# Optimization experiments

Measured on AMD Instinct MI355X. Metric: run time of the kernel, lower is better.

Reference implementation:

```python
import jax, jax.numpy as jnp
import numpy as np

NMAX = 8
LMAX = 3
RC = 5.0
SIGMA = 0.5
SMOOTH_W = 0.5
N_SPECIES = 4
N_ATOMS = 20000
N_EDGES = 800000
LMMAX = (LMAX + 1) ** 2  # 16
# map each (l,m) flat index to its l (block structure of mult_ln_lm)
LM_TO_L = jnp.asarray(np.repeat(np.arange(LMAX + 1), 2 * np.arange(LMAX + 1) + 1))


def real_sph_harm_l3(d):
    """Real spherical harmonics, integral normalization, l=0..3. d: [J,3] unit vectors."""
    x, y, z = d[:, 0], d[:, 1], d[:, 2]
    x2, y2, z2 = x * x, y * y, z * z
    cols = [
        jnp.full_like(x, 0.28209479177387814),                 # l=0
        0.4886025119029199 * y,                                # l=1, m=-1
        0.4886025119029199 * z,                                # l=1, m=0
        0.4886025119029199 * x,                                # l=1, m=1
        1.0925484305920792 * x * y,                            # l=2, m=-2
        1.0925484305920792 * y * z,                            # l=2, m=-1
        0.31539156525252005 * (2.0 * z2 - x2 - y2),            # l=2, m=0
        1.0925484305920792 * x * z,                            # l=2, m=1
        0.5462742152960396 * (x2 - y2),                        # l=2, m=2
        0.5900435899266435 * y * (3.0 * x2 - y2),              # l=3, m=-3
        2.890611442640554 * x * y * z,                         # l=3, m=-2
        0.4570457994644658 * y * (4.0 * z2 - x2 - y2),         # l=3, m=-1
        0.3731763325901154 * z * (2.0 * z2 - 3.0 * x2 - 3.0 * y2),  # l=3, m=0
        0.4570457994644658 * x * (4.0 * z2 - x2 - y2),         # l=3, m=1
        1.445305721320277 * z * (x2 - y2),                     # l=3, m=2
        0.5900435899266435 * x * (x2 - 3.0 * y2),              # l=3, m=3
    ]
    return jnp.stack(cols, axis=-1)  # [J, 16]


def shifted_cosine_cutoff(r):
    """f=1 for r<rc-w, smooth cosine decay to 0 at rc, 0 beyond."""
    w = SMOOTH_W
    t = 0.5 * (1.0 + jnp.cos(jnp.pi * jnp.clip((r - (RC - w)) / w, 0.0, 1.0)))
    return jnp.where(r < RC - w, 1.0, jnp.where(r < RC, t, 0.0))


def setup_inputs() -> dict:
    key = jax.random.key(0)
    k1, k2, k3, k4, k5, k6 = jax.random.split(key, 6)
    distances = jax.random.uniform(k1, (N_EDGES,), jnp.float32, 0.05, RC * 0.999)
    dv = jax.random.normal(k2, (N_EDGES, 3), jnp.float32)
    direction_vectors = dv / jnp.linalg.norm(dv, axis=1, keepdims=True)
    radial_centers = jax.random.uniform(k3, ((LMAX + 1) * NMAX,), jnp.float32, 0.0, RC)
    z = jax.random.randint(k4, (N_ATOMS,), 0, N_SPECIES)
    idx_i = jax.random.randint(k5, (N_EDGES,), 0, N_ATOMS)
    idx_j = jax.random.randint(k6, (N_EDGES,), 0, N_ATOMS)
    return {"distances": distances, "direction_vectors": direction_vectors,
            "radial_centers": radial_centers, "z": z, "idx_i": idx_i, "idx_j": idx_j}


def reference(distances, direction_vectors, radial_centers, z, idx_i, idx_j):
    J = distances.shape[0]
    # spherical harmonics of edge directions: [J, lmmax]
    Ylm = real_sph_harm_l3(direction_vectors)
    # radial integrals (Gaussian-basis spline surrogate) * cutoff: [J, lmax+1, nmax]
    rb = jnp.exp(-0.5 * jnp.square((distances[:, None] - radial_centers[None, :]) / SIGMA))
    RIln = rb.reshape(J, LMAX + 1, NMAX) * shifted_cosine_cutoff(distances)[:, None, None]
    # block-wise outer product (vectorized mult_ln_lm): [J, nmax, lmmax]
    cij_nlm = RIln[:, LM_TO_L, :].transpose(0, 2, 1) * Ylm[:, None, :]
    # species- and atom-dependent scatter-add
    reduction_ids = z[idx_j] + N_SPECIES * idx_i
    ci = jax.ops.segment_sum(cij_nlm.reshape(J, -1), reduction_ids,
                             num_segments=N_SPECIES * N_ATOMS)
    return ci.reshape(N_ATOMS, N_SPECIES, NMAX, LMMAX)
```

## Files before the change

kernel.cpp:

```cpp
#include <hip/hip_runtime.h>
#include <math.h>


#define NSPEC 4
#define CAP   32

typedef float v2f __attribute__((ext_vector_type(2)));

__constant__ float YCOEF[16 * 20] = {
    0.28209479177387814f,0,0,0, 0,0,0,0, 0,0,0,0, 0,0,0,0, 0,0,0,0,
    0,0,0.4886025119029199f,0, 0,0,0,0, 0,0,0,0, 0,0,0,0, 0,0,0,0,
    0,0,0,0.4886025119029199f, 0,0,0,0, 0,0,0,0, 0,0,0,0, 0,0,0,0,
    0,0.4886025119029199f,0,0, 0,0,0,0, 0,0,0,0, 0,0,0,0, 0,0,0,0,
    0,0,0,0, 0,0,0,1.0925484305920792f, 0,0,0,0, 0,0,0,0, 0,0,0,0,
    0,0,0,0, 0,0,0,0, 0,1.0925484305920792f,0,0, 0,0,0,0, 0,0,0,0,
    0,0,0,0, -0.31539156525252005f,-0.31539156525252005f,0.6307831305050401f,0, 0,0,0,0, 0,0,0,0, 0,0,0,0,
    0,0,0,0, 0,0,0,0, 1.0925484305920792f,0,0,0, 0,0,0,0, 0,0,0,0,
    0,0,0,0, 0.5462742152960396f,-0.5462742152960396f,0,0, 0,0,0,0, 0,0,0,0, 0,0,0,0,
    0,0,0,0, 0,0,0,0, 0,0,0,1.7701307697799305f, 0,0,0,0, -0.5900435899266435f,0,0,0,
    0,0,0,0, 0,0,0,0, 0,0,0,0, 0,0,2.890611442640554f,0, 0,0,0,0,
    0,0,0,0, 0,0,0,0, 0,0,0,-0.4570457994644658f, 0,0,0,0, -0.4570457994644658f,0,1.8281831978578632f,0,
    0,0,0,0, 0,0,0,0, 0,0,0,0, -1.1195289977703462f,0,0,0, 0,-1.1195289977703462f,0,0.7463526651802308f,
    0,0,0,0, 0,0,0,0, 0,0,-0.4570457994644658f,0, 0,-0.4570457994644658f,0,1.8281831978578632f, 0,0,0,0,
    0,0,0,0, 0,0,0,0, 0,0,0,0, 1.445305721320277f,0,0,0, 0,-1.445305721320277f,0,0,
    0,0,0,0, 0,0,0,0, 0,0,0.5900435899266435f,0, 0,-1.7701307697799305f,0,0, 0,0,0,0,
};

__device__ __forceinline__ void gather_row(
    const float4* __restrict__ payload, const float* __restrict__ centers,
    float* __restrict__ out, int row, int lane, int beg, int end, int clampHi)
{
    int q = lane >> 4;
    int t = lane & 15;
    int l = (t >= 9) ? 3 : (t >= 4) ? 2 : (t >= 1) ? 1 : 0;
    float cenA = centers[2 * t];
    float cenB = centers[2 * t + 1];
    int srcA = (q << 4) + (l << 2);

    const float4* cr = (const float4*)(&YCOEF[t * 20]);
    float4 c0 = cr[0], c1 = cr[1], c2 = cr[2], c3 = cr[3], c4 = cr[4];
    v2f K0 = {c0.x, c0.y}, K1 = {c0.z, c0.w};
    v2f K2 = {c1.x, c1.y}, K3 = {c1.z, c1.w};
    v2f K4 = {c2.x, c2.y}, K5 = {c2.z, c2.w};
    v2f K6 = {c3.x, c3.y}, K7 = {c3.z, c3.w};
    v2f K8 = {c4.x, c4.y}, K9 = {c4.z, c4.w};
    asm volatile("" : "+v"(K0), "+v"(K1), "+v"(K2), "+v"(K3), "+v"(K4),
                      "+v"(K5), "+v"(K6), "+v"(K7), "+v"(K8), "+v"(K9),
                      "+v"(cenA), "+v"(cenB));

    v2f A0 = {0, 0}, A1 = {0, 0}, A2 = {0, 0}, A3 = {0, 0};

    if (beg < end) {
        float4 P = payload[beg];
        for (int i = beg; i < end; ++i) {
            int nx = i + 1 < clampHi ? i + 1 : clampHi;
            float4 Pn = payload[nx];
            float x = P.x, y = P.y, z = P.z, r = P.w;

            float xx = x * x, yy = y * y, zz = z * z;
            v2f m0 = {1.0f, x};
            v2f m1 = {y, z};
            v2f m2 = {xx, yy};
            v2f m3 = {zz, x * y};
            v2f m4 = {x * z, y * z};
            v2f m5 = {xx * x, xx * y};
            v2f m6 = {xx * z, x * yy};
            v2f m7 = {x * y * z, x * zz};
            v2f m8 = {yy * y, yy * z};
            v2f m9 = {y * zz, zz * z};

            v2f pa = K0 * m0 + K1 * m1;
            v2f pb = K2 * m2 + K3 * m3;
            pa += K4 * m4;
            pb += K5 * m5;
            pa += K6 * m6;
            pb += K7 * m7;
            pa += K8 * m8;
            pb += K9 * m9;
            v2f ps = pa + pb;
            float ylm = ps.x + ps.y;

            float u  = fminf(fmaxf((r - 4.5f) * 2.0f, 0.0f), 1.0f);
            float fc = fmaf(0.5f, __cosf(3.14159265358979f * u), 0.5f);
            float p  = fc * ylm;

            float dA = r - cenA;
            float dB = r - cenB;
            float rb0 = __expf(-2.0f * dA * dA);
            float rb1 = __expf(-2.0f * dB * dB);

            float b0 = __shfl(rb0, srcA,     64);
            float b1 = __shfl(rb1, srcA,     64);
            float b2 = __shfl(rb0, srcA + 1, 64);
            float b3 = __shfl(rb1, srcA + 1, 64);
            float b4 = __shfl(rb0, srcA + 2, 64);
            float b5 = __shfl(rb1, srcA + 2, 64);
            float b6 = __shfl(rb0, srcA + 3, 64);
            float b7 = __shfl(rb1, srcA + 3, 64);

            v2f pp = {p, p};
            A0 += pp * (v2f){b0, b1};
            A1 += pp * (v2f){b2, b3};
            A2 += pp * (v2f){b4, b5};
            A3 += pp * (v2f){b6, b7};
            P = Pn;
        }
    }

    float* o = out + (size_t)row * 128 + t;
    o[0]   = A0.x; o[16]  = A0.y; o[32]  = A1.x; o[48]  = A1.y;
    o[64]  = A2.x; o[80]  = A2.y; o[96]  = A3.x; o[112] = A3.y;
}

__global__ __launch_bounds__(256) void k_scatter_direct(
    const float* __restrict__ dist, const float* __restrict__ dirs,
    const int* __restrict__ zsp, const int* __restrict__ idx_i,
    const int* __restrict__ idx_j,
    int* __restrict__ cnt, float4* __restrict__ payload, int J)
{
    int e = blockIdx.x * 256 + threadIdx.x;
    if (e >= J) return;
    int rid = zsp[idx_j[e]] + NSPEC * idx_i[e];
    int pos = atomicAdd(&cnt[rid], 1);
    if (pos < CAP) {
        float4 v;
        v.x = dirs[3 * e + 0];
        v.y = dirs[3 * e + 1];
        v.z = dirs[3 * e + 2];
        v.w = dist[e];
        payload[(size_t)rid * CAP + pos] = v;
    }
}

__global__ __launch_bounds__(256) void k_gather_big(
    const float4* __restrict__ payload, const float* __restrict__ centers,
    const int* __restrict__ cnt, float* __restrict__ out, int nrows)
{
    int wave = threadIdx.x >> 6;
    int lane = threadIdx.x & 63;
    int row = blockIdx.x * 16 + wave * 4 + (lane >> 4);
    if (row >= nrows) return;
    int c = cnt[row];
    c = c < CAP ? c : CAP;
    int beg = row * CAP;
    gather_row(payload, centers, out, row, lane, beg, beg + c, beg + CAP - 1);
}

__global__ __launch_bounds__(256) void k_hist(
    const int* __restrict__ zsp, const int* __restrict__ idx_i,
    const int* __restrict__ idx_j, int* __restrict__ counts, int J)
{
    int e = blockIdx.x * 256 + threadIdx.x;
    if (e >= J) return;
    atomicAdd(&counts[zsp[idx_j[e]] + NSPEC * idx_i[e]], 1);
}

__global__ __launch_bounds__(256) void k_scan1(
    const int* __restrict__ counts, int* __restrict__ cursor,
    int* __restrict__ bsums, int n)
{
    __shared__ int s[256];
    int i = blockIdx.x * 256 + threadIdx.x;
    int v = (i < n) ? counts[i] : 0;
    s[threadIdx.x] = v;
    __syncthreads();
    for (int off = 1; off < 256; off <<= 1) {
        int t = (threadIdx.x >= off) ? s[threadIdx.x - off] : 0;
        __syncthreads();
        s[threadIdx.x] += t;
        __syncthreads();
    }
    if (i < n) cursor[i] = s[threadIdx.x] - v;
    if (threadIdx.x == 255) bsums[blockIdx.x] = s[255];
}

__global__ __launch_bounds__(512) void k_scan2(int* __restrict__ bsums, int nb)
{
    __shared__ int s[512];
    int t = threadIdx.x;
    int v = (t < nb) ? bsums[t] : 0;
    s[t] = v;
    __syncthreads();
    for (int off = 1; off < 512; off <<= 1) {
        int u = (t >= off) ? s[t - off] : 0;
        __syncthreads();
        s[t] += u;
        __syncthreads();
    }
    if (t < nb) bsums[t] = s[t] - v;
}

__global__ __launch_bounds__(256) void k_scatter(
    const float* __restrict__ dist, const float* __restrict__ dirs,
    const int* __restrict__ zsp, const int* __restrict__ idx_i,
    const int* __restrict__ idx_j,
    int* __restrict__ cursor, const int* __restrict__ bsums,
    float4* __restrict__ payload, int J)
{
    int e = blockIdx.x * 256 + threadIdx.x;
    if (e >= J) return;
    int rid = zsp[idx_j[e]] + NSPEC * idx_i[e];
    int pos = bsums[rid >> 8] + atomicAdd(&cursor[rid], 1);
    float4 v;
    v.x = dirs[3 * e + 0];
    v.y = dirs[3 * e + 1];
    v.z = dirs[3 * e + 2];
    v.w = dist[e];
    payload[pos] = v;
}

__global__ __launch_bounds__(256) void k_gather_small(
    const float4* __restrict__ payload, const float* __restrict__ centers,
    const int* __restrict__ cursor, const int* __restrict__ bsums,
    float* __restrict__ out, int nrows, int J)
{
    int wave = threadIdx.x >> 6;
    int lane = threadIdx.x & 63;
    int row = blockIdx.x * 16 + wave * 4 + (lane >> 4);
    if (row >= nrows) return;
    int end = bsums[row >> 8] + cursor[row];
    int beg = (row == 0) ? 0 : bsums[(row - 1) >> 8] + cursor[row - 1];
    gather_row(payload, centers, out, row, lane, beg, end, J - 1);
}

__global__ __launch_bounds__(256) void sphexp16_fb(
    const float* __restrict__ dist, const float* __restrict__ dirs,
    const float* __restrict__ centers, const int* __restrict__ zsp,
    const int* __restrict__ idx_i, const int* __restrict__ idx_j,
    float* __restrict__ out, int J)
{
    int tid = blockIdx.x * 256 + threadIdx.x;
    int e = tid >> 4, t = tid & 15;
    if (e >= J) return;
    float r = dist[e];
    float x = dirs[3*e], y = dirs[3*e+1], z = dirs[3*e+2];
    int rid = zsp[idx_j[e]] + NSPEC * idx_i[e];
    size_t base = (size_t)rid * 128 + t;
    const float* cr = &YCOEF[t * 20];
    float xx=x*x, yy=y*y, zz=z*z;
    float ylm = cr[0] + cr[1]*x + cr[2]*y + cr[3]*z
              + cr[4]*xx + cr[5]*yy + cr[6]*zz + cr[7]*(x*y)
              + cr[8]*(x*z) + cr[9]*(y*z)
              + cr[10]*(xx*x) + cr[11]*(xx*y) + cr[12]*(xx*z)
              + cr[13]*(x*yy) + cr[14]*(x*y*z) + cr[15]*(x*zz)
              + cr[16]*(yy*y) + cr[17]*(yy*z) + cr[18]*(y*zz) + cr[19]*(zz*z);
    float u = fminf(fmaxf((r - 4.5f) * 2.0f, 0.0f), 1.0f);
    float fc = 0.5f * (1.0f + __cosf(3.14159265358979f * u));
    int l = (t >= 9) ? 3 : (t >= 4) ? 2 : (t >= 1) ? 1 : 0;
    float pref = fc * ylm;
#pragma unroll
    for (int n = 0; n < 8; n++) {
        float d = r - centers[l*8+n];
        atomicAdd(out + base + (size_t)(n*16), pref * __expf(-2.0f*d*d));
    }
}

extern "C" void kernel_launch(void* const* d_in, const int* in_sizes, int n_in,
                              void* d_out, int out_size, void* d_ws, size_t ws_size,
                              hipStream_t stream) {
    const float* dist    = (const float*)d_in[0];
    const float* dirs    = (const float*)d_in[1];
    const float* centers = (const float*)d_in[2];
    const int*   zsp     = (const int*)d_in[3];
    const int*   idx_i   = (const int*)d_in[4];
    const int*   idx_j   = (const int*)d_in[5];
    float* out = (float*)d_out;

    int J      = in_sizes[0];
    int natoms = in_sizes[3];
    int nrows  = natoms * NSPEC;
    int nb1    = (nrows + 255) / 256;

    size_t need_big   = (size_t)nrows * CAP * 16 + (size_t)nrows * 4;
    size_t need_small = (size_t)J * 16 + (2 * (size_t)nrows + 512) * 4;

    if (ws_size >= need_big) {
        float4* payload = (float4*)d_ws;
        int* cnt = (int*)(payload + (size_t)nrows * CAP);
        hipMemsetAsync(cnt, 0, (size_t)nrows * sizeof(int), stream);
        k_scatter_direct<<<(J + 255) / 256, 256, 0, stream>>>(
            dist, dirs, zsp, idx_i, idx_j, cnt, payload, J);
        k_gather_big<<<(nrows + 15) / 16, 256, 0, stream>>>(
            payload, centers, cnt, out, nrows);
    } else if (ws_size >= need_small && nb1 <= 512) {
        float4* payload = (float4*)d_ws;
        int* counts = (int*)(payload + J);
        int* cursor = counts + nrows;
        int* bsums  = cursor + nrows;
        hipMemsetAsync(counts, 0, (size_t)nrows * sizeof(int), stream);
        k_hist<<<(J + 255) / 256, 256, 0, stream>>>(zsp, idx_i, idx_j, counts, J);
        k_scan1<<<nb1, 256, 0, stream>>>(counts, cursor, bsums, nrows);
        k_scan2<<<1, 512, 0, stream>>>(bsums, nb1);
        k_scatter<<<(J + 255) / 256, 256, 0, stream>>>(
            dist, dirs, zsp, idx_i, idx_j, cursor, bsums, payload, J);
        k_gather_small<<<(nrows + 15) / 16, 256, 0, stream>>>(
            payload, centers, cursor, bsums, out, nrows, J);
    } else {
        hipMemsetAsync(d_out, 0, (size_t)out_size * sizeof(float), stream);
        long long total = (long long)J * 16;
        sphexp16_fb<<<(int)((total + 255) / 256), 256, 0, stream>>>(
            dist, dirs, centers, zsp, idx_i, idx_j, out, J);
    }
}
```

Measured before the change: 163.5 us.

## Split each row's edges across four lane groups and vectorize the scatter loads

The gather kernel now gives each output row a whole wave: four 16-lane groups each handle every fourth edge of the row, and the partial sums are reduced with cross-lane xor shuffles before one group writes the result. This cuts the serial per-row loop length by about four, which matters because rows hold roughly ten edges on average and the old loop was latency-bound. The cost is four times as many waves plus the shuffle reduction and masked padding work. The scatter kernel now has each thread process four edges with vectorized int4/float4 loads of indices, distances and directions, reducing the number of load instructions.

```diff
diff --git a/kernel.cpp b/kernel.cpp
--- a/kernel.cpp
+++ b/kernel.cpp
@@ -28,7 +28,7 @@
 
 __device__ __forceinline__ void gather_row(
     const float4* __restrict__ payload, const float* __restrict__ centers,
-    float* __restrict__ out, int row, int lane, int beg, int end, int clampHi)
+    float* __restrict__ out, int row, int lane, int beg, int end)
 {
     int q = lane >> 4;
     int t = lane & 15;
@@ -50,24 +50,34 @@
 
     v2f A0 = {0, 0}, A1 = {0, 0}, A2 = {0, 0}, A3 = {0, 0};
 
-    if (beg < end) {
-        float4 P = payload[beg];
-        for (int i = beg; i < end; ++i) {
-            int nx = i + 1 < clampHi ? i + 1 : clampHi;
-            float4 Pn = payload[nx];
-            float x = P.x, y = P.y, z = P.z, r = P.w;
-
-            float xx = x * x, yy = y * y, zz = z * z;
+    int cnt = end - beg;
+    if (cnt > 0) {
+        int last = end - 1;
+        int slot = beg + q;
+        float4 P = payload[slot < end ? slot : last];
+        bool val = slot < end;
+        int iters = (cnt + 3) >> 2;
+        for (int it = 0; it < iters; ++it) {
+            int nslot = slot + 4;
+            float4 Pn = payload[nslot < end ? nslot : last];
+            bool nval = nslot < end;
+
+            float x  = val ? P.x : 0.0f;
+            float y  = val ? P.y : 0.0f;
+            float zc = val ? P.z : 0.0f;
+            float r  = val ? P.w : 10.0f;
+
+            float xx = x * x, yy = y * y, zz = zc * zc;
             v2f m0 = {1.0f, x};
-            v2f m1 = {y, z};
+            v2f m1 = {y, zc};
             v2f m2 = {xx, yy};
             v2f m3 = {zz, x * y};
-            v2f m4 = {x * z, y * z};
+            v2f m4 = {x * zc, y * zc};
             v2f m5 = {xx * x, xx * y};
-            v2f m6 = {xx * z, x * yy};
-            v2f m7 = {x * y * z, x * zz};
-            v2f m8 = {yy * y, yy * z};
-            v2f m9 = {y * zz, zz * z};
+            v2f m6 = {xx * zc, x * yy};
+            v2f m7 = {x * y * zc, x * zz};
+            v2f m8 = {yy * y, yy * zc};
+            v2f m9 = {y * zz, zz * zc};
 
             v2f pa = K0 * m0 + K1 * m1;
             v2f pb = K2 * m2 + K3 * m3;
@@ -103,13 +113,25 @@
             A1 += pp * (v2f){b2, b3};
             A2 += pp * (v2f){b4, b5};
             A3 += pp * (v2f){b6, b7};
-            P = Pn;
+
+            P = Pn; val = nval; slot = nslot;
         }
     }
 
-    float* o = out + (size_t)row * 128 + t;
-    o[0]   = A0.x; o[16]  = A0.y; o[32]  = A1.x; o[48]  = A1.y;
-    o[64]  = A2.x; o[80]  = A2.y; o[96]  = A3.x; o[112] = A3.y;
+    A0.x += __shfl_xor(A0.x, 16, 64); A0.x += __shfl_xor(A0.x, 32, 64);
+    A0.y += __shfl_xor(A0.y, 16, 64); A0.y += __shfl_xor(A0.y, 32, 64);
+    A1.x += __shfl_xor(A1.x, 16, 64); A1.x += __shfl_xor(A1.x, 32, 64);
+    A1.y += __shfl_xor(A1.y, 16, 64); A1.y += __shfl_xor(A1.y, 32, 64);
+    A2.x += __shfl_xor(A2.x, 16, 64); A2.x += __shfl_xor(A2.x, 32, 64);
+    A2.y += __shfl_xor(A2.y, 16, 64); A2.y += __shfl_xor(A2.y, 32, 64);
+    A3.x += __shfl_xor(A3.x, 16, 64); A3.x += __shfl_xor(A3.x, 32, 64);
+    A3.y += __shfl_xor(A3.y, 16, 64); A3.y += __shfl_xor(A3.y, 32, 64);
+
+    if (q == 0) {
+        float* o = out + (size_t)row * 128 + t;
+        o[0]   = A0.x; o[16]  = A0.y; o[32]  = A1.x; o[48]  = A1.y;
+        o[64]  = A2.x; o[80]  = A2.y; o[96]  = A3.x; o[112] = A3.y;
+    }
 }
 
 __global__ __launch_bounds__(256) void k_scatter_direct(
@@ -118,17 +140,42 @@
     const int* __restrict__ idx_j,
     int* __restrict__ cnt, float4* __restrict__ payload, int J)
 {
-    int e = blockIdx.x * 256 + threadIdx.x;
-    if (e >= J) return;
-    int rid = zsp[idx_j[e]] + NSPEC * idx_i[e];
-    int pos = atomicAdd(&cnt[rid], 1);
-    if (pos < CAP) {
-        float4 v;
-        v.x = dirs[3 * e + 0];
-        v.y = dirs[3 * e + 1];
-        v.z = dirs[3 * e + 2];
-        v.w = dist[e];
-        payload[(size_t)rid * CAP + pos] = v;
+    int tid = blockIdx.x * 256 + threadIdx.x;
+    int e0 = tid * 4;
+    if (e0 >= J) return;
+    if (e0 + 4 <= J) {
+        int4 ji = *(const int4*)(idx_j + e0);
+        int4 ii = *(const int4*)(idx_i + e0);
+        int z0 = zsp[ji.x], z1 = zsp[ji.y], z2 = zsp[ji.z], z3 = zsp[ji.w];
+        float4 d  = *(const float4*)(dist + e0);
+        float4 u0 = *(const float4*)(dirs + 3 * e0);
+        float4 u1 = *(const float4*)(dirs + 3 * e0 + 4);
+        float4 u2 = *(const float4*)(dirs + 3 * e0 + 8);
+        int r0 = z0 + NSPEC * ii.x;
+        int r1 = z1 + NSPEC * ii.y;
+        int r2 = z2 + NSPEC * ii.z;
+        int r3 = z3 + NSPEC * ii.w;
+        int p0 = atomicAdd(&cnt[r0], 1);
+        int p1 = atomicAdd(&cnt[r1], 1);
+        int p2 = atomicAdd(&cnt[r2], 1);
+        int p3 = atomicAdd(&cnt[r3], 1);
+        if (p0 < CAP) payload[(size_t)r0 * CAP + p0] = make_float4(u0.x, u0.y, u0.z, d.x);
+        if (p1 < CAP) payload[(size_t)r1 * CAP + p1] = make_float4(u0.w, u1.x, u1.y, d.y);
+        if (p2 < CAP) payload[(size_t)r2 * CAP + p2] = make_float4(u1.z, u1.w, u2.x, d.z);
+        if (p3 < CAP) payload[(size_t)r3 * CAP + p3] = make_float4(u2.y, u2.z, u2.w, d.w);
+    } else {
+        for (int e = e0; e < J; ++e) {
+            int rid = zsp[idx_j[e]] + NSPEC * idx_i[e];
+            int pos = atomicAdd(&cnt[rid], 1);
+            if (pos < CAP) {
+                float4 v;
+                v.x = dirs[3 * e + 0];
+                v.y = dirs[3 * e + 1];
+                v.z = dirs[3 * e + 2];
+                v.w = dist[e];
+                payload[(size_t)rid * CAP + pos] = v;
+            }
+        }
     }
 }
 
@@ -138,12 +185,12 @@
 {
     int wave = threadIdx.x >> 6;
     int lane = threadIdx.x & 63;
-    int row = blockIdx.x * 16 + wave * 4 + (lane >> 4);
+    int row = blockIdx.x * 4 + wave;
     if (row >= nrows) return;
     int c = cnt[row];
     c = c < CAP ? c : CAP;
     int beg = row * CAP;
-    gather_row(payload, centers, out, row, lane, beg, beg + c, beg + CAP - 1);
+    gather_row(payload, centers, out, row, lane, beg, beg + c);
 }
 
 __global__ __launch_bounds__(256) void k_hist(
@@ -212,15 +259,15 @@
 __global__ __launch_bounds__(256) void k_gather_small(
     const float4* __restrict__ payload, const float* __restrict__ centers,
     const int* __restrict__ cursor, const int* __restrict__ bsums,
-    float* __restrict__ out, int nrows, int J)
+    float* __restrict__ out, int nrows)
 {
     int wave = threadIdx.x >> 6;
     int lane = threadIdx.x & 63;
-    int row = blockIdx.x * 16 + wave * 4 + (lane >> 4);
+    int row = blockIdx.x * 4 + wave;
     if (row >= nrows) return;
     int end = bsums[row >> 8] + cursor[row];
     int beg = (row == 0) ? 0 : bsums[(row - 1) >> 8] + cursor[row - 1];
-    gather_row(payload, centers, out, row, lane, beg, end, J - 1);
+    gather_row(payload, centers, out, row, lane, beg, end);
 }
 
 __global__ __launch_bounds__(256) void sphexp16_fb(
@@ -278,9 +325,10 @@
         float4* payload = (float4*)d_ws;
         int* cnt = (int*)(payload + (size_t)nrows * CAP);
         hipMemsetAsync(cnt, 0, (size_t)nrows * sizeof(int), stream);
-        k_scatter_direct<<<(J + 255) / 256, 256, 0, stream>>>(
+        int nthread = (J + 3) / 4;
+        k_scatter_direct<<<(nthread + 255) / 256, 256, 0, stream>>>(
             dist, dirs, zsp, idx_i, idx_j, cnt, payload, J);
-        k_gather_big<<<(nrows + 15) / 16, 256, 0, stream>>>(
+        k_gather_big<<<(nrows + 3) / 4, 256, 0, stream>>>(
             payload, centers, cnt, out, nrows);
     } else if (ws_size >= need_small && nb1 <= 512) {
         float4* payload = (float4*)d_ws;
@@ -293,8 +341,8 @@
         k_scan2<<<1, 512, 0, stream>>>(bsums, nb1);
         k_scatter<<<(J + 255) / 256, 256, 0, stream>>>(
             dist, dirs, zsp, idx_i, idx_j, cursor, bsums, payload, J);
-        k_gather_small<<<(nrows + 15) / 16, 256, 0, stream>>>(
-            payload, centers, cursor, bsums, out, nrows, J);
+        k_gather_small<<<(nrows + 3) / 4, 256, 0, stream>>>(
+            payload, centers, cursor, bsums, out, nrows);
     } else {
         hipMemsetAsync(d_out, 0, (size_t)out_size * sizeof(float), stream);
         long long total = (long long)J * 16;
```

After: 180.1 us. 1.1x slower.

## Store edge index and distance in payload, split row edges across wave quarters

Applied to the files above, without the earlier changes.

The scatter pass now writes an 8-byte payload (edge index bit-cast to float, plus distance) instead of a 16-byte float4 holding the direction and distance. The gather kernel reads directions indirectly from the input array, and rows get a whole wave instead of a quarter wave. Each 16-lane quarter handles every fourth edge, and partial sums are combined with xor shuffles before the store. This halves the scatter write and payload read traffic and shortens per-row serial loops, at the cost of an indirect random gather for directions, cross-lane reductions, and four times more blocks.

```diff
diff --git a/kernel.cpp b/kernel.cpp
--- a/kernel.cpp
+++ b/kernel.cpp
@@ -27,8 +27,9 @@
 };
 
 __device__ __forceinline__ void gather_row(
-    const float4* __restrict__ payload, const float* __restrict__ centers,
-    float* __restrict__ out, int row, int lane, int beg, int end, int clampHi)
+    const float2* __restrict__ payload, const float* __restrict__ dirs,
+    const float* __restrict__ centers, float* __restrict__ out,
+    int row, int lane, int beg, int end)
 {
     int q = lane >> 4;
     int t = lane & 15;
@@ -50,24 +51,58 @@
 
     v2f A0 = {0, 0}, A1 = {0, 0}, A2 = {0, 0}, A3 = {0, 0};
 
-    if (beg < end) {
-        float4 P = payload[beg];
-        for (int i = beg; i < end; ++i) {
-            int nx = i + 1 < clampHi ? i + 1 : clampHi;
-            float4 Pn = payload[nx];
-            float x = P.x, y = P.y, z = P.z, r = P.w;
-
-            float xx = x * x, yy = y * y, zz = z * z;
-            v2f m0 = {1.0f, x};
-            v2f m1 = {y, z};
+    int cnt = end - beg;
+    if (cnt > 0) {
+        int last = end - 1;
+        int slot = beg + q;
+        int c0s = slot < end ? slot : last;
+        int c1s = slot + 4 < end ? slot + 4 : last;
+        float2 B0 = payload[c0s];
+        float2 B1 = payload[c1s];
+        int e0 = __float_as_int(B0.x);
+        float x  = dirs[3 * e0 + 0];
+        float y  = dirs[3 * e0 + 1];
+        float zc = dirs[3 * e0 + 2];
+        int iters = (cnt + 3) >> 2;
+        for (int it = 0; it < iters; ++it) {
+            int s2 = slot + 8;
+            float2 B2 = payload[s2 < end ? s2 : last];
+            int e1 = __float_as_int(B1.x);
+            float xn = dirs[3 * e1 + 0];
+            float yn = dirs[3 * e1 + 1];
+            float zn = dirs[3 * e1 + 2];
+
+            bool v = slot < end;
+            float xm = v ? x    : 0.0f;
+            float ym = v ? y    : 0.0f;
+            float zm = v ? zc   : 0.0f;
+            float rm = v ? B0.y : 10.0f;
+
+            float dA = rm - cenA;
+            float dB = rm - cenB;
+            float rb0 = __expf(-2.0f * dA * dA);
+            float rb1 = __expf(-2.0f * dB * dB);
+
+            float b0 = __shfl(rb0, srcA,     64);
+            float b1 = __shfl(rb1, srcA,     64);
+            float b2 = __shfl(rb0, srcA + 1, 64);
+            float b3 = __shfl(rb1, srcA + 1, 64);
+            float b4 = __shfl(rb0, srcA + 2, 64);
+            float b5 = __shfl(rb1, srcA + 2, 64);
+            float b6 = __shfl(rb0, srcA + 3, 64);
+            float b7 = __shfl(rb1, srcA + 3, 64);
+
+            float xx = xm * xm, yy = ym * ym, zz = zm * zm;
+            v2f m0 = {1.0f, xm};
+            v2f m1 = {ym, zm};
             v2f m2 = {xx, yy};
-            v2f m3 = {zz, x * y};
-            v2f m4 = {x * z, y * z};
-            v2f m5 = {xx * x, xx * y};
-            v2f m6 = {xx * z, x * yy};
-            v2f m7 = {x * y * z, x * zz};
-            v2f m8 = {yy * y, yy * z};
-            v2f m9 = {y * zz, zz * z};
+            v2f m3 = {zz, xm * ym};
+            v2f m4 = {xm * zm, ym * zm};
+            v2f m5 = {xx * xm, xx * ym};
+            v2f m6 = {xx * zm, xm * yy};
+            v2f m7 = {xm * ym * zm, xm * zz};
+            v2f m8 = {yy * ym, yy * zm};
+            v2f m9 = {ym * zz, zz * zm};
 
             v2f pa = K0 * m0 + K1 * m1;
             v2f pb = K2 * m2 + K3 * m3;
@@ -80,70 +115,75 @@
             v2f ps = pa + pb;
             float ylm = ps.x + ps.y;
 
-            float u  = fminf(fmaxf((r - 4.5f) * 2.0f, 0.0f), 1.0f);
+            float u  = fminf(fmaxf((rm - 4.5f) * 2.0f, 0.0f), 1.0f);
             float fc = fmaf(0.5f, __cosf(3.14159265358979f * u), 0.5f);
             float p  = fc * ylm;
-
-            float dA = r - cenA;
-            float dB = r - cenB;
-            float rb0 = __expf(-2.0f * dA * dA);
-            float rb1 = __expf(-2.0f * dB * dB);
-
-            float b0 = __shfl(rb0, srcA,     64);
-            float b1 = __shfl(rb1, srcA,     64);
-            float b2 = __shfl(rb0, srcA + 1, 64);
-            float b3 = __shfl(rb1, srcA + 1, 64);
-            float b4 = __shfl(rb0, srcA + 2, 64);
-            float b5 = __shfl(rb1, srcA + 2, 64);
-            float b6 = __shfl(rb0, srcA + 3, 64);
-            float b7 = __shfl(rb1, srcA + 3, 64);
 
             v2f pp = {p, p};
             A0 += pp * (v2f){b0, b1};
             A1 += pp * (v2f){b2, b3};
             A2 += pp * (v2f){b4, b5};
             A3 += pp * (v2f){b6, b7};
-            P = Pn;
+
+            B0 = B1; B1 = B2;
+            x = xn; y = yn; zc = zn;
+            slot += 4;
         }
     }
 
-    float* o = out + (size_t)row * 128 + t;
-    o[0]   = A0.x; o[16]  = A0.y; o[32]  = A1.x; o[48]  = A1.y;
-    o[64]  = A2.x; o[80]  = A2.y; o[96]  = A3.x; o[112] = A3.y;
+    A0.x += __shfl_xor(A0.x, 16, 64); A0.x += __shfl_xor(A0.x, 32, 64);
+    A0.y += __shfl_xor(A0.y, 16, 64); A0.y += __shfl_xor(A0.y, 32, 64);
+    A1.x += __shfl_xor(A1.x, 16, 64); A1.x += __shfl_xor(A1.x, 32, 64);
+    A1.y += __shfl_xor(A1.y, 16, 64); A1.y += __shfl_xor(A1.y, 32, 64);
+    A2.x += __shfl_xor(A2.x, 16, 64); A2.x += __shfl_xor(A2.x, 32, 64);
+    A2.y += __shfl_xor(A2.y, 16, 64); A2.y += __shfl_xor(A2.y, 32, 64);
+    A3.x += __shfl_xor(A3.x, 16, 64); A3.x += __shfl_xor(A3.x, 32, 64);
+    A3.y += __shfl_xor(A3.y, 16, 64); A3.y += __shfl_xor(A3.y, 32, 64);
+
+    float w0, w1;
+    switch (q) {
+        case 0: w0 = A0.x; w1 = A0.y; break;
+        case 1: w0 = A1.x; w1 = A1.y; break;
+        case 2: w0 = A2.x; w1 = A2.y; break;
+        default: w0 = A3.x; w1 = A3.y; break;
+    }
+    float* o = out + (size_t)row * 128;
+    o[32 * q + t]      = w0;
+    o[32 * q + 16 + t] = w1;
 }
 
 __global__ __launch_bounds__(256) void k_scatter_direct(
-    const float* __restrict__ dist, const float* __restrict__ dirs,
+    const float* __restrict__ dist,
     const int* __restrict__ zsp, const int* __restrict__ idx_i,
     const int* __restrict__ idx_j,
-    int* __restrict__ cnt, float4* __restrict__ payload, int J)
+    int* __restrict__ cnt, float2* __restrict__ payload, int J)
 {
     int e = blockIdx.x * 256 + threadIdx.x;
     if (e >= J) return;
     int rid = zsp[idx_j[e]] + NSPEC * idx_i[e];
+    float r = dist[e];
     int pos = atomicAdd(&cnt[rid], 1);
     if (pos < CAP) {
-        float4 v;
-        v.x = dirs[3 * e + 0];
-        v.y = dirs[3 * e + 1];
-        v.z = dirs[3 * e + 2];
-        v.w = dist[e];
-        payload[(size_t)rid * CAP + pos] = v;
+        float2 v;
+        v.x = __int_as_float(e);
+        v.y = r;
+        payload[rid * CAP + pos] = v;
     }
 }
 
 __global__ __launch_bounds__(256) void k_gather_big(
-    const float4* __restrict__ payload, const float* __restrict__ centers,
+    const float2* __restrict__ payload, const float* __restrict__ dirs,
+    const float* __restrict__ centers,
     const int* __restrict__ cnt, float* __restrict__ out, int nrows)
 {
     int wave = threadIdx.x >> 6;
     int lane = threadIdx.x & 63;
-    int row = blockIdx.x * 16 + wave * 4 + (lane >> 4);
+    int row = blockIdx.x * 4 + wave;
     if (row >= nrows) return;
     int c = cnt[row];
     c = c < CAP ? c : CAP;
     int beg = row * CAP;
-    gather_row(payload, centers, out, row, lane, beg, beg + c, beg + CAP - 1);
+    gather_row(payload, dirs, centers, out, row, lane, beg, beg + c);
 }
 
 __global__ __launch_bounds__(256) void k_hist(
@@ -191,36 +231,35 @@
 }
 
 __global__ __launch_bounds__(256) void k_scatter(
-    const float* __restrict__ dist, const float* __restrict__ dirs,
+    const float* __restrict__ dist,
     const int* __restrict__ zsp, const int* __restrict__ idx_i,
     const int* __restrict__ idx_j,
     int* __restrict__ cursor, const int* __restrict__ bsums,
-    float4* __restrict__ payload, int J)
+    float2* __restrict__ payload, int J)
 {
     int e = blockIdx.x * 256 + threadIdx.x;
     if (e >= J) return;
     int rid = zsp[idx_j[e]] + NSPEC * idx_i[e];
     int pos = bsums[rid >> 8] + atomicAdd(&cursor[rid], 1);
-    float4 v;
-    v.x = dirs[3 * e + 0];
-    v.y = dirs[3 * e + 1];
-    v.z = dirs[3 * e + 2];
-    v.w = dist[e];
+    float2 v;
+    v.x = __int_as_float(e);
+    v.y = dist[e];
     payload[pos] = v;
 }
 
 __global__ __launch_bounds__(256) void k_gather_small(
-    const float4* __restrict__ payload, const float* __restrict__ centers,
+    const float2* __restrict__ payload, const float* __restrict__ dirs,
+    const float* __restrict__ centers,
     const int* __restrict__ cursor, const int* __restrict__ bsums,
-    float* __restrict__ out, int nrows, int J)
+    float* __restrict__ out, int nrows)
 {
     int wave = threadIdx.x >> 6;
     int lane = threadIdx.x & 63;
-    int row = blockIdx.x * 16 + wave * 4 + (lane >> 4);
+    int row = blockIdx.x * 4 + wave;
     if (row >= nrows) return;
     int end = bsums[row >> 8] + cursor[row];
     int beg = (row == 0) ? 0 : bsums[(row - 1) >> 8] + cursor[row - 1];
-    gather_row(payload, centers, out, row, lane, beg, end, J - 1);
+    gather_row(payload, dirs, centers, out, row, lane, beg, end);
 }
 
 __global__ __launch_bounds__(256) void sphexp16_fb(
@@ -271,19 +310,19 @@
     int nrows  = natoms * NSPEC;
     int nb1    = (nrows + 255) / 256;
 
-    size_t need_big   = (size_t)nrows * CAP * 16 + (size_t)nrows * 4;
-    size_t need_small = (size_t)J * 16 + (2 * (size_t)nrows + 512) * 4;
+    size_t need_big   = (size_t)nrows * CAP * 8 + (size_t)nrows * 4;
+    size_t need_small = (size_t)J * 8 + (2 * (size_t)nrows + 512) * 4;
 
     if (ws_size >= need_big) {
-        float4* payload = (float4*)d_ws;
+        float2* payload = (float2*)d_ws;
         int* cnt = (int*)(payload + (size_t)nrows * CAP);
         hipMemsetAsync(cnt, 0, (size_t)nrows * sizeof(int), stream);
         k_scatter_direct<<<(J + 255) / 256, 256, 0, stream>>>(
-            dist, dirs, zsp, idx_i, idx_j, cnt, payload, J);
-        k_gather_big<<<(nrows + 15) / 16, 256, 0, stream>>>(
-            payload, centers, cnt, out, nrows);
+            dist, zsp, idx_i, idx_j, cnt, payload, J);
+        k_gather_big<<<(nrows + 3) / 4, 256, 0, stream>>>(
+            payload, dirs, centers, cnt, out, nrows);
     } else if (ws_size >= need_small && nb1 <= 512) {
-        float4* payload = (float4*)d_ws;
+        float2* payload = (float2*)d_ws;
         int* counts = (int*)(payload + J);
         int* cursor = counts + nrows;
         int* bsums  = cursor + nrows;
@@ -292,9 +331,9 @@
         k_scan1<<<nb1, 256, 0, stream>>>(counts, cursor, bsums, nrows);
         k_scan2<<<1, 512, 0, stream>>>(bsums, nb1);
         k_scatter<<<(J + 255) / 256, 256, 0, stream>>>(
-            dist, dirs, zsp, idx_i, idx_j, cursor, bsums, payload, J);
-        k_gather_small<<<(nrows + 15) / 16, 256, 0, stream>>>(
-            payload, centers, cursor, bsums, out, nrows, J);
+            dist, zsp, idx_i, idx_j, cursor, bsums, payload, J);
+        k_gather_small<<<(nrows + 3) / 4, 256, 0, stream>>>(
+            payload, dirs, centers, cursor, bsums, out, nrows);
     } else {
         hipMemsetAsync(d_out, 0, (size_t)out_size * sizeof(float), stream);
         long long total = (long long)J * 16;
```

New measurement: 176.3 us. 7.8% more time.

## Process two edges per iteration and compute all eight radials per lane without shuffles

Applied to the files above, without the earlier changes.

The gather loop now handles two edges per iteration using packed float2 math. Each lane computes all eight Gaussian radial terms for its own l block directly, which removes the eight cross-lane shuffles per edge; the old scheme shared two exp values per lane. This raises the exp count per lane from two to eight per edge, and the two-edge accumulators are summed at the end. The early return is replaced by a guarded store so inactive rows still join the loop safely.

```diff
diff --git a/kernel.cpp b/kernel.cpp
--- a/kernel.cpp
+++ b/kernel.cpp
@@ -26,90 +26,99 @@
     0,0,0,0, 0,0,0,0, 0,0,0.5900435899266435f,0, 0,-1.7701307697799305f,0,0, 0,0,0,0,
 };
 
-__device__ __forceinline__ void gather_row(
-    const float4* __restrict__ payload, const float* __restrict__ centers,
-    float* __restrict__ out, int row, int lane, int beg, int end, int clampHi)
-{
-    int q = lane >> 4;
+__device__ __forceinline__ void gather4_body(
+    const float4* __restrict__ pay, const float* __restrict__ centers,
+    float* __restrict__ out, int nrows, int row, int lane, int beg, int end)
+{
     int t = lane & 15;
     int l = (t >= 9) ? 3 : (t >= 4) ? 2 : (t >= 1) ? 1 : 0;
-    float cenA = centers[2 * t];
-    float cenB = centers[2 * t + 1];
-    int srcA = (q << 4) + (l << 2);
-
-    const float4* cr = (const float4*)(&YCOEF[t * 20]);
-    float4 c0 = cr[0], c1 = cr[1], c2 = cr[2], c3 = cr[3], c4 = cr[4];
-    v2f K0 = {c0.x, c0.y}, K1 = {c0.z, c0.w};
-    v2f K2 = {c1.x, c1.y}, K3 = {c1.z, c1.w};
-    v2f K4 = {c2.x, c2.y}, K5 = {c2.z, c2.w};
-    v2f K6 = {c3.x, c3.y}, K7 = {c3.z, c3.w};
-    v2f K8 = {c4.x, c4.y}, K9 = {c4.z, c4.w};
+
+    const float* cr = &YCOEF[t * 20];
+    float K0 = cr[0],  K1 = cr[1],  K2 = cr[2],  K3 = cr[3],  K4 = cr[4];
+    float K5 = cr[5],  K6 = cr[6],  K7 = cr[7],  K8 = cr[8],  K9 = cr[9];
+    float K10 = cr[10], K11 = cr[11], K12 = cr[12], K13 = cr[13], K14 = cr[14];
+    float K15 = cr[15], K16 = cr[16], K17 = cr[17], K18 = cr[18], K19 = cr[19];
+    const float* cb = centers + 8 * l;
+    float C0 = cb[0], C1 = cb[1], C2 = cb[2], C3 = cb[3];
+    float C4 = cb[4], C5 = cb[5], C6 = cb[6], C7 = cb[7];
     asm volatile("" : "+v"(K0), "+v"(K1), "+v"(K2), "+v"(K3), "+v"(K4),
-                      "+v"(K5), "+v"(K6), "+v"(K7), "+v"(K8), "+v"(K9),
-                      "+v"(cenA), "+v"(cenB));
-
-    v2f A0 = {0, 0}, A1 = {0, 0}, A2 = {0, 0}, A3 = {0, 0};
+                      "+v"(K5), "+v"(K6), "+v"(K7), "+v"(K8), "+v"(K9));
+    asm volatile("" : "+v"(K10), "+v"(K11), "+v"(K12), "+v"(K13), "+v"(K14),
+                      "+v"(K15), "+v"(K16), "+v"(K17), "+v"(K18), "+v"(K19));
+    asm volatile("" : "+v"(C0), "+v"(C1), "+v"(C2), "+v"(C3),
+                      "+v"(C4), "+v"(C5), "+v"(C6), "+v"(C7));
+
+    v2f A0 = {0,0}, A1 = {0,0}, A2 = {0,0}, A3 = {0,0};
+    v2f A4 = {0,0}, A5 = {0,0}, A6 = {0,0}, A7 = {0,0};
 
     if (beg < end) {
-        float4 P = payload[beg];
-        for (int i = beg; i < end; ++i) {
-            int nx = i + 1 < clampHi ? i + 1 : clampHi;
-            float4 Pn = payload[nx];
-            float x = P.x, y = P.y, z = P.z, r = P.w;
-
-            float xx = x * x, yy = y * y, zz = z * z;
-            v2f m0 = {1.0f, x};
-            v2f m1 = {y, z};
-            v2f m2 = {xx, yy};
-            v2f m3 = {zz, x * y};
-            v2f m4 = {x * z, y * z};
-            v2f m5 = {xx * x, xx * y};
-            v2f m6 = {xx * z, x * yy};
-            v2f m7 = {x * y * z, x * zz};
-            v2f m8 = {yy * y, yy * z};
-            v2f m9 = {y * zz, zz * z};
-
-            v2f pa = K0 * m0 + K1 * m1;
-            v2f pb = K2 * m2 + K3 * m3;
-            pa += K4 * m4;
-            pb += K5 * m5;
-            pa += K6 * m6;
-            pb += K7 * m7;
-            pa += K8 * m8;
-            pb += K9 * m9;
-            v2f ps = pa + pb;
-            float ylm = ps.x + ps.y;
-
-            float u  = fminf(fmaxf((r - 4.5f) * 2.0f, 0.0f), 1.0f);
-            float fc = fmaf(0.5f, __cosf(3.14159265358979f * u), 0.5f);
-            float p  = fc * ylm;
-
-            float dA = r - cenA;
-            float dB = r - cenB;
-            float rb0 = __expf(-2.0f * dA * dA);
-            float rb1 = __expf(-2.0f * dB * dB);
-
-            float b0 = __shfl(rb0, srcA,     64);
-            float b1 = __shfl(rb1, srcA,     64);
-            float b2 = __shfl(rb0, srcA + 1, 64);
-            float b3 = __shfl(rb1, srcA + 1, 64);
-            float b4 = __shfl(rb0, srcA + 2, 64);
-            float b5 = __shfl(rb1, srcA + 2, 64);
-            float b6 = __shfl(rb0, srcA + 3, 64);
-            float b7 = __shfl(rb1, srcA + 3, 64);
-
-            v2f pp = {p, p};
-            A0 += pp * (v2f){b0, b1};
-            A1 += pp * (v2f){b2, b3};
-            A2 += pp * (v2f){b4, b5};
-            A3 += pp * (v2f){b6, b7};
-            P = Pn;
+        int last = end - 1;
+        float4 Pa = pay[beg];
+        int ib = (beg + 1 < end) ? beg + 1 : last;
+        float4 Pb = pay[ib];
+        for (int i = beg; i < end; i += 2) {
+            int na = (i + 2 < end) ? i + 2 : last;
+            int nb = (i + 3 < end) ? i + 3 : last;
+            float4 Na = pay[na];
+            float4 Nb = pay[nb];
+
+            v2f xp = {Pa.x, Pb.x};
+            v2f yp = {Pa.y, Pb.y};
+            v2f zp = {Pa.z, Pb.z};
+            v2f rp = {Pa.w, Pb.w};
+
+            v2f xx = xp * xp, yy = yp * yp, zz = zp * zp;
+            v2f xy = xp * yp, xz = xp * zp, yz = yp * zp;
+
+            v2f a = (v2f){K0, K0} + xp * K1;
+            v2f b = yp * K2 + zp * K3;
+            a += xx * K4;           b += yy * K5;
+            a += zz * K6;           b += xy * K7;
+            a += xz * K8;           b += yz * K9;
+            a += (xx * xp) * K10;   b += (xx * yp) * K11;
+            a += (xx * zp) * K12;   b += (xp * yy) * K13;
+            a += (xy * zp) * K14;   b += (xp * zz) * K15;
+            a += (yy * yp) * K16;   b += (yy * zp) * K17;
+            a += (yp * zz) * K18;   b += (zz * zp) * K19;
+            v2f ylm = a + b;
+
+            v2f u = rp * 2.0f + (v2f){-9.0f, -9.0f};
+            u.x = fminf(fmaxf(u.x, 0.0f), 1.0f);
+            u.y = fminf(fmaxf(u.y, 0.0f), 1.0f);
+            float f0 = __cosf(3.14159265358979f * u.x);
+            float f1 = __cosf(3.14159265358979f * u.y);
+            v2f fcp = {fmaf(0.5f, f0, 0.5f), fmaf(0.5f, f1, 0.5f)};
+            v2f p = fcp * ylm;
+            p.y = (i + 1 < end) ? p.y : 0.0f;
+            v2f d, rb;
+            d = rp - C0; d = d * d;
+            rb.x = __expf(-2.0f * d.x); rb.y = __expf(-2.0f * d.y); A0 += p * rb;
+            d = rp - C1; d = d * d;
+            rb.x = __expf(-2.0f * d.x); rb.y = __expf(-2.0f * d.y); A1 += p * rb;
+            d = rp - C2; d = d * d;
+            rb.x = __expf(-2.0f * d.x); rb.y = __expf(-2.0f * d.y); A2 += p * rb;
+            d = rp - C3; d = d * d;
+            rb.x = __expf(-2.0f * d.x); rb.y = __expf(-2.0f * d.y); A3 += p * rb;
+            d = rp - C4; d = d * d;
+            rb.x = __expf(-2.0f * d.x); rb.y = __expf(-2.0f * d.y); A4 += p * rb;
+            d = rp - C5; d = d * d;
+            rb.x = __expf(-2.0f * d.x); rb.y = __expf(-2.0f * d.y); A5 += p * rb;
+            d = rp - C6; d = d * d;
+            rb.x = __expf(-2.0f * d.x); rb.y = __expf(-2.0f * d.y); A6 += p * rb;
+            d = rp - C7; d = d * d;
+            rb.x = __expf(-2.0f * d.x); rb.y = __expf(-2.0f * d.y); A7 += p * rb;
+
+            Pa = Na; Pb = Nb;
         }
     }
 
-    float* o = out + (size_t)row * 128 + t;
-    o[0]   = A0.x; o[16]  = A0.y; o[32]  = A1.x; o[48]  = A1.y;
-    o[64]  = A2.x; o[80]  = A2.y; o[96]  = A3.x; o[112] = A3.y;
+    if (row < nrows) {
+        float* o = out + (size_t)row * 128 + t;
+        o[0]   = A0.x + A0.y; o[16]  = A1.x + A1.y;
+        o[32]  = A2.x + A2.y; o[48]  = A3.x + A3.y;
+        o[64]  = A4.x + A4.y; o[80]  = A5.x + A5.y;
+        o[96]  = A6.x + A6.y; o[112] = A7.x + A7.y;
+    }
 }
 
 __global__ __launch_bounds__(256) void k_scatter_direct(
@@ -133,17 +142,17 @@
 }
 
 __global__ __launch_bounds__(256) void k_gather_big(
-    const float4* __restrict__ payload, const float* __restrict__ centers,
+    const float4* __restrict__ pay, const float* __restrict__ centers,
     const int* __restrict__ cnt, float* __restrict__ out, int nrows)
 {
     int wave = threadIdx.x >> 6;
     int lane = threadIdx.x & 63;
     int row = blockIdx.x * 16 + wave * 4 + (lane >> 4);
-    if (row >= nrows) return;
-    int c = cnt[row];
+    int c = 0;
+    if (row < nrows) c = cnt[row];
     c = c < CAP ? c : CAP;
     int beg = row * CAP;
-    gather_row(payload, centers, out, row, lane, beg, beg + c, beg + CAP - 1);
+    gather4_body(pay, centers, out, nrows, row, lane, beg, beg + c);
 }
 
 __global__ __launch_bounds__(256) void k_hist(
@@ -210,17 +219,19 @@
 }
 
 __global__ __launch_bounds__(256) void k_gather_small(
-    const float4* __restrict__ payload, const float* __restrict__ centers,
+    const float4* __restrict__ pay, const float* __restrict__ centers,
     const int* __restrict__ cursor, const int* __restrict__ bsums,
-    float* __restrict__ out, int nrows, int J)
+    float* __restrict__ out, int nrows)
 {
     int wave = threadIdx.x >> 6;
     int lane = threadIdx.x & 63;
     int row = blockIdx.x * 16 + wave * 4 + (lane >> 4);
-    if (row >= nrows) return;
-    int end = bsums[row >> 8] + cursor[row];
-    int beg = (row == 0) ? 0 : bsums[(row - 1) >> 8] + cursor[row - 1];
-    gather_row(payload, centers, out, row, lane, beg, end, J - 1);
+    int beg = 0, end = 0;
+    if (row < nrows) {
+        end = bsums[row >> 8] + cursor[row];
+        beg = (row == 0) ? 0 : bsums[(row - 1) >> 8] + cursor[row - 1];
+    }
+    gather4_body(pay, centers, out, nrows, row, lane, beg, end);
 }
 
 __global__ __launch_bounds__(256) void sphexp16_fb(
@@ -274,13 +285,15 @@
     size_t need_big   = (size_t)nrows * CAP * 16 + (size_t)nrows * 4;
     size_t need_small = (size_t)J * 16 + (2 * (size_t)nrows + 512) * 4;
 
+    int gblocks = (nrows + 15) / 16;
+
     if (ws_size >= need_big) {
         float4* payload = (float4*)d_ws;
         int* cnt = (int*)(payload + (size_t)nrows * CAP);
         hipMemsetAsync(cnt, 0, (size_t)nrows * sizeof(int), stream);
         k_scatter_direct<<<(J + 255) / 256, 256, 0, stream>>>(
             dist, dirs, zsp, idx_i, idx_j, cnt, payload, J);
-        k_gather_big<<<(nrows + 15) / 16, 256, 0, stream>>>(
+        k_gather_big<<<gblocks, 256, 0, stream>>>(
             payload, centers, cnt, out, nrows);
     } else if (ws_size >= need_small && nb1 <= 512) {
         float4* payload = (float4*)d_ws;
@@ -293,8 +306,8 @@
         k_scan2<<<1, 512, 0, stream>>>(bsums, nb1);
         k_scatter<<<(J + 255) / 256, 256, 0, stream>>>(
             dist, dirs, zsp, idx_i, idx_j, cursor, bsums, payload, J);
-        k_gather_small<<<(nrows + 15) / 16, 256, 0, stream>>>(
-            payload, centers, cursor, bsums, out, nrows, J);
+        k_gather_small<<<gblocks, 256, 0, stream>>>(
+            payload, centers, cursor, bsums, out, nrows);
     } else {
         hipMemsetAsync(d_out, 0, (size_t)out_size * sizeof(float), stream);
         long long total = (long long)J * 16;
```

Result: slower. 174.4 us (+6.6%).
